# Optimization experiments

Hardware: AMD Instinct MI355X
Metric: run time of the kernel (lower is better)

## Reference

```python
import jax, jax.numpy as jnp
import numpy as np

NUM_TYPES = 4  # unique atom types, e.g. H,C,N,O
N_DESC = 384   # descriptor width (nDescriptors())


def setup_inputs() -> dict:
    key = jax.random.key(0)
    k1, k2, k3 = jax.random.split(key, 3)
    n_confs, n_atoms = 2048, 64
    coords = jax.random.normal(k1, (n_confs, n_atoms, 3), dtype=jnp.float32)
    atom_types = jax.random.randint(k2, (n_confs, n_atoms), 0, NUM_TYPES, dtype=jnp.int64)
    W = jax.random.normal(k3, (3, N_DESC), dtype=jnp.float32)
    return {"coords": coords, "atom_types": atom_types, "W": W}


def reference(coords, atom_types, W):
    n_confs, n_atoms, _ = coords.shape
    # stub descriptor computer: per-atom descriptor, (n_confs*n_atoms, N_DESC)
    desc = jnp.tanh(coords.reshape(-1, 3) @ W)
    at2type = atom_types.reshape(-1)                      # (N,)
    # conformer index for every atom: [0,0,...,0,1,1,...]
    at2conf = jnp.repeat(jnp.arange(n_confs, dtype=jnp.int64), n_atoms)
    # stable sort by atom type (routing permutation)
    perm = jnp.argsort(at2type, stable=True)              # (N,)
    desc_sorted = desc[perm]                              # gather (N, N_DESC)
    at2conf_sorted = at2conf[perm]                        # (N,)
    at_type_count = jnp.bincount(at2type, length=NUM_TYPES)  # split sizes per type
    # per-type buckets = desc_sorted split at cumsum(at_type_count); returned
    # concatenated with counts to keep shapes static under jit.
    return desc_sorted, at2conf_sorted, at_type_count
```

## Files before the change

### kernel.cpp

```cpp
#include <hip/hip_runtime.h>

#define NDESC 384
#define NTYPES 4
#define BLOCK_ATOMS 256
#define NTHREADS 384

typedef unsigned int uint32;
typedef unsigned long long u64;
typedef float f4 __attribute__((ext_vector_type(4)));

__device__ __forceinline__ float fast_tanh(float x) {
  float e = __builtin_amdgcn_exp2f(x * 2.8853900817779268f);
  return 1.0f - 2.0f * __builtin_amdgcn_rcpf(1.0f + e);
}

__global__ __launch_bounds__(BLOCK_ATOMS) void hist_kernel(
    const int* __restrict__ types, uint32* __restrict__ blockHist, int n) {
  __shared__ uint32 waveCnt[BLOCK_ATOMS / 64][NTYPES];
  int tid = threadIdx.x;
  int idx = blockIdx.x * BLOCK_ATOMS + tid;
  int ty = (idx < n) ? types[idx] : -1;
  int wave = tid >> 6, lane = tid & 63;
  for (int t = 0; t < NTYPES; ++t) {
    u64 m = __ballot(ty == t);
    if (lane == 0) waveCnt[wave][t] = (uint32)__popcll(m);
  }
  __syncthreads();
  if (tid < NTYPES) {
    uint32 s = 0;
    for (int w = 0; w < BLOCK_ATOMS / 64; ++w) s += waveCnt[w][tid];
    blockHist[blockIdx.x * NTYPES + tid] = s;
  }
}

__global__ __launch_bounds__(NTHREADS) void main_kernel(
    const float* __restrict__ coords, const int* __restrict__ types,
    const float* __restrict__ W, const uint32* __restrict__ blockHist,
    float* __restrict__ descOut, float* __restrict__ confOut,
    float* __restrict__ countsOut, int n, int nb) {
  __shared__ float sW[3 * NDESC];
  __shared__ float sC[BLOCK_ATOMS][3];
  __shared__ uint32 sRankPos[BLOCK_ATOMS];
  __shared__ uint32 sRankAtom[BLOCK_ATOMS];
  __shared__ uint32 waveCnt[BLOCK_ATOMS / 64][NTYPES];
  __shared__ uint32 sTot[NTYPES];
  __shared__ uint32 sOff[NTYPES];
  __shared__ uint32 sCum[NTYPES];

  int tid = threadIdx.x;
  int bid = blockIdx.x;
  int base = bid * BLOCK_ATOMS;

  for (int i = tid; i < 3 * NDESC; i += NTHREADS) sW[i] = W[i];
  for (int i = tid; i < BLOCK_ATOMS * 3; i += NTHREADS) {
    int g = base * 3 + i;
    sC[i / 3][i % 3] = (g < n * 3) ? coords[g] : 0.0f;
  }

  int idx = base + tid;
  int ty = -1;
  if (tid < BLOCK_ATOMS && idx < n) ty = types[idx];
  int wave = tid >> 6, lane = tid & 63;
  int myrank = 0;
  if (tid < BLOCK_ATOMS) {
    for (int t = 0; t < NTYPES; ++t) {
      u64 m = __ballot(ty == t);
      if (lane == 0) waveCnt[wave][t] = (uint32)__popcll(m);
      if (t == ty) myrank = (int)__popcll(m & ((1ull << lane) - 1ull));
    }
  }

  if (wave < NTYPES) {
    int t = wave;
    uint32 tot = 0, pre = 0;
    for (int b = lane; b < nb; b += 64) {
      uint32 h = blockHist[b * NTYPES + t];
      tot += h;
      if (b < bid) pre += h;
    }
    for (int off = 32; off > 0; off >>= 1) {
      tot += __shfl_down(tot, off);
      pre += __shfl_down(pre, off);
    }
    if (lane == 0) { sTot[t] = tot; sOff[t] = pre; }
  }
  __syncthreads();
  if (tid == 0) {
    uint32 b = 0, c = 0;
    for (int t = 0; t < NTYPES; ++t) {
      sOff[t] += b;
      b += sTot[t];
      uint32 cnt = 0;
      for (int w = 0; w < BLOCK_ATOMS / 64; ++w) cnt += waveCnt[w][t];
      sCum[t] = c;
      c += cnt;
    }
  }
  if (bid == 0 && tid < NTYPES) countsOut[tid] = (float)sTot[tid];
  __syncthreads();

  if (tid < BLOCK_ATOMS && ty >= 0) {
    uint32 fullrank = (uint32)myrank;
    for (int w = 0; w < wave; ++w) fullrank += waveCnt[w][ty];
    uint32 pos = sOff[ty] + fullrank;
    uint32 brk = sCum[ty] + fullrank;
    sRankPos[brk] = pos;
    sRankAtom[brk] = (uint32)tid;
    confOut[pos] = (float)(idx >> 6);
  }
  __syncthreads();

  int r = tid / 96;
  int c = tid - r * 96;
  int d0 = 4 * c;
  float w00 = sW[d0], w01 = sW[d0 + 1], w02 = sW[d0 + 2], w03 = sW[d0 + 3];
  float w10 = sW[NDESC + d0], w11 = sW[NDESC + d0 + 1],
        w12 = sW[NDESC + d0 + 2], w13 = sW[NDESC + d0 + 3];
  float w20 = sW[2 * NDESC + d0], w21 = sW[2 * NDESC + d0 + 1],
        w22 = sW[2 * NDESC + d0 + 2], w23 = sW[2 * NDESC + d0 + 3];

  int valid = n - base;
  if (valid > BLOCK_ATOMS) valid = BLOCK_ATOMS;

  if (valid == BLOCK_ATOMS) {
#pragma unroll 8
    for (int k0 = 0; k0 < BLOCK_ATOMS; k0 += 4) {
      int k = k0 + r;
      uint32 a = sRankAtom[k];
      uint32 pos = sRankPos[k];
      float c0 = sC[a][0], c1 = sC[a][1], c2 = sC[a][2];
      f4 v;
      v.x = fast_tanh(c0 * w00 + c1 * w10 + c2 * w20);
      v.y = fast_tanh(c0 * w01 + c1 * w11 + c2 * w21);
      v.z = fast_tanh(c0 * w02 + c1 * w12 + c2 * w22);
      v.w = fast_tanh(c0 * w03 + c1 * w13 + c2 * w23);
      __builtin_nontemporal_store(
          v, reinterpret_cast<f4*>(descOut + (size_t)pos * NDESC + d0));
    }
  } else {
    for (int k0 = 0; k0 < BLOCK_ATOMS; k0 += 4) {
      int k = k0 + r;
      if (k < valid) {
        uint32 a = sRankAtom[k];
        uint32 pos = sRankPos[k];
        float c0 = sC[a][0], c1 = sC[a][1], c2 = sC[a][2];
        f4 v;
        v.x = fast_tanh(c0 * w00 + c1 * w10 + c2 * w20);
        v.y = fast_tanh(c0 * w01 + c1 * w11 + c2 * w21);
        v.z = fast_tanh(c0 * w02 + c1 * w12 + c2 * w22);
        v.w = fast_tanh(c0 * w03 + c1 * w13 + c2 * w23);
        __builtin_nontemporal_store(
            v, reinterpret_cast<f4*>(descOut + (size_t)pos * NDESC + d0));
      }
    }
  }
}

extern "C" void kernel_launch(void* const* d_in, const int* in_sizes, int n_in,
                              void* d_out, int out_size, void* d_ws, size_t ws_size,
                              hipStream_t stream) {
  const float* coords = (const float*)d_in[0];
  const int* types = (const int*)d_in[1];
  const float* W = (const float*)d_in[2];

  int n = in_sizes[1];
  int nb = (n + BLOCK_ATOMS - 1) / BLOCK_ATOMS;

  uint32* blockHist = (uint32*)d_ws;

  float* descOut = (float*)d_out;
  float* confOut = descOut + (size_t)n * NDESC;
  float* countsOut = confOut + n;

  hipLaunchKernelGGL(hist_kernel, dim3(nb), dim3(BLOCK_ATOMS), 0, stream,
                     types, blockHist, n);
  hipLaunchKernelGGL(main_kernel, dim3(nb), dim3(NTHREADS), 0, stream,
                     coords, types, W, blockHist, descOut, confOut, countsOut,
                     n, nb);
}
```

Baseline: 53.71 us.

## Split scatter into permutation kernel plus contiguous gather-compute kernel

```diff
diff --git a/kernel.cpp b/kernel.cpp
--- a/kernel.cpp
+++ b/kernel.cpp
@@ -4,6 +4,7 @@
 #define NTYPES 4
 #define BLOCK_ATOMS 256
 #define NTHREADS 384
+#define ROWS 64
 
 typedef unsigned int uint32;
 typedef unsigned long long u64;
@@ -33,41 +34,24 @@
   }
 }
 
-__global__ __launch_bounds__(NTHREADS) void main_kernel(
-    const float* __restrict__ coords, const int* __restrict__ types,
-    const float* __restrict__ W, const uint32* __restrict__ blockHist,
-    float* __restrict__ descOut, float* __restrict__ confOut,
-    float* __restrict__ countsOut, int n, int nb) {
-  __shared__ float sW[3 * NDESC];
-  __shared__ float sC[BLOCK_ATOMS][3];
-  __shared__ uint32 sRankPos[BLOCK_ATOMS];
-  __shared__ uint32 sRankAtom[BLOCK_ATOMS];
+__global__ __launch_bounds__(BLOCK_ATOMS) void perm_kernel(
+    const int* __restrict__ types, const uint32* __restrict__ blockHist,
+    uint32* __restrict__ perm, float* __restrict__ countsOut, int n, int nb) {
   __shared__ uint32 waveCnt[BLOCK_ATOMS / 64][NTYPES];
   __shared__ uint32 sTot[NTYPES];
   __shared__ uint32 sOff[NTYPES];
-  __shared__ uint32 sCum[NTYPES];
 
   int tid = threadIdx.x;
   int bid = blockIdx.x;
   int base = bid * BLOCK_ATOMS;
-
-  for (int i = tid; i < 3 * NDESC; i += NTHREADS) sW[i] = W[i];
-  for (int i = tid; i < BLOCK_ATOMS * 3; i += NTHREADS) {
-    int g = base * 3 + i;
-    sC[i / 3][i % 3] = (g < n * 3) ? coords[g] : 0.0f;
-  }
-
   int idx = base + tid;
-  int ty = -1;
-  if (tid < BLOCK_ATOMS && idx < n) ty = types[idx];
+  int ty = (idx < n) ? types[idx] : -1;
   int wave = tid >> 6, lane = tid & 63;
   int myrank = 0;
-  if (tid < BLOCK_ATOMS) {
-    for (int t = 0; t < NTYPES; ++t) {
-      u64 m = __ballot(ty == t);
-      if (lane == 0) waveCnt[wave][t] = (uint32)__popcll(m);
-      if (t == ty) myrank = (int)__popcll(m & ((1ull << lane) - 1ull));
-    }
+  for (int t = 0; t < NTYPES; ++t) {
+    u64 m = __ballot(ty == t);
+    if (lane == 0) waveCnt[wave][t] = (uint32)__popcll(m);
+    if (t == ty) myrank = (int)__popcll(m & ((1ull << lane) - 1ull));
   }
 
   if (wave < NTYPES) {
@@ -86,27 +70,42 @@
   }
   __syncthreads();
   if (tid == 0) {
-    uint32 b = 0, c = 0;
-    for (int t = 0; t < NTYPES; ++t) {
-      sOff[t] += b;
-      b += sTot[t];
-      uint32 cnt = 0;
-      for (int w = 0; w < BLOCK_ATOMS / 64; ++w) cnt += waveCnt[w][t];
-      sCum[t] = c;
-      c += cnt;
-    }
+    uint32 b = 0;
+    for (int t = 0; t < NTYPES; ++t) { sOff[t] += b; b += sTot[t]; }
   }
   if (bid == 0 && tid < NTYPES) countsOut[tid] = (float)sTot[tid];
   __syncthreads();
 
-  if (tid < BLOCK_ATOMS && ty >= 0) {
+  if (ty >= 0) {
     uint32 fullrank = (uint32)myrank;
     for (int w = 0; w < wave; ++w) fullrank += waveCnt[w][ty];
-    uint32 pos = sOff[ty] + fullrank;
-    uint32 brk = sCum[ty] + fullrank;
-    sRankPos[brk] = pos;
-    sRankAtom[brk] = (uint32)tid;
-    confOut[pos] = (float)(idx >> 6);
+    perm[sOff[ty] + fullrank] = (uint32)idx;
+  }
+}
+
+__global__ __launch_bounds__(NTHREADS) void gather_kernel(
+    const float* __restrict__ coords, const uint32* __restrict__ perm,
+    const float* __restrict__ W, float* __restrict__ descOut,
+    float* __restrict__ confOut, int n) {
+  __shared__ float sW[3 * NDESC];
+  __shared__ float sC[ROWS][3];
+  __shared__ uint32 sPerm[ROWS];
+
+  int tid = threadIdx.x;
+  int base = blockIdx.x * ROWS;
+
+  for (int i = tid; i < 3 * NDESC; i += NTHREADS) sW[i] = W[i];
+  if (tid < ROWS) {
+    int p = base + tid;
+    uint32 a = (p < n) ? perm[p] : 0u;
+    sPerm[tid] = a;
+    if (p < n) confOut[p] = (float)(a >> 6);
+  }
+  __syncthreads();
+  if (tid < ROWS * 3) {
+    int rrow = tid / 3, comp = tid - 3 * rrow;
+    sC[rrow][comp] = (base + rrow < n)
+                         ? coords[(size_t)sPerm[rrow] * 3 + comp] : 0.0f;
   }
   __syncthreads();
 
@@ -120,37 +119,31 @@
         w22 = sW[2 * NDESC + d0 + 2], w23 = sW[2 * NDESC + d0 + 3];
 
   int valid = n - base;
-  if (valid > BLOCK_ATOMS) valid = BLOCK_ATOMS;
+  if (valid > ROWS) valid = ROWS;
 
-  if (valid == BLOCK_ATOMS) {
-#pragma unroll 8
-    for (int k0 = 0; k0 < BLOCK_ATOMS; k0 += 4) {
+  if (valid == ROWS) {
+#pragma unroll 4
+    for (int k0 = 0; k0 < ROWS; k0 += 4) {
       int k = k0 + r;
-      uint32 a = sRankAtom[k];
-      uint32 pos = sRankPos[k];
-      float c0 = sC[a][0], c1 = sC[a][1], c2 = sC[a][2];
+      float c0 = sC[k][0], c1 = sC[k][1], c2 = sC[k][2];
       f4 v;
       v.x = fast_tanh(c0 * w00 + c1 * w10 + c2 * w20);
       v.y = fast_tanh(c0 * w01 + c1 * w11 + c2 * w21);
       v.z = fast_tanh(c0 * w02 + c1 * w12 + c2 * w22);
       v.w = fast_tanh(c0 * w03 + c1 * w13 + c2 * w23);
-      __builtin_nontemporal_store(
-          v, reinterpret_cast<f4*>(descOut + (size_t)pos * NDESC + d0));
+      *reinterpret_cast<f4*>(descOut + (size_t)(base + k) * NDESC + d0) = v;
     }
   } else {
-    for (int k0 = 0; k0 < BLOCK_ATOMS; k0 += 4) {
+    for (int k0 = 0; k0 < ROWS; k0 += 4) {
       int k = k0 + r;
       if (k < valid) {
-        uint32 a = sRankAtom[k];
-        uint32 pos = sRankPos[k];
-        float c0 = sC[a][0], c1 = sC[a][1], c2 = sC[a][2];
+        float c0 = sC[k][0], c1 = sC[k][1], c2 = sC[k][2];
         f4 v;
         v.x = fast_tanh(c0 * w00 + c1 * w10 + c2 * w20);
         v.y = fast_tanh(c0 * w01 + c1 * w11 + c2 * w21);
         v.z = fast_tanh(c0 * w02 + c1 * w12 + c2 * w22);
         v.w = fast_tanh(c0 * w03 + c1 * w13 + c2 * w23);
-        __builtin_nontemporal_store(
-            v, reinterpret_cast<f4*>(descOut + (size_t)pos * NDESC + d0));
+        *reinterpret_cast<f4*>(descOut + (size_t)(base + k) * NDESC + d0) = v;
       }
     }
   }
@@ -165,8 +158,10 @@
 
   int n = in_sizes[1];
   int nb = (n + BLOCK_ATOMS - 1) / BLOCK_ATOMS;
+  int ngb = (n + ROWS - 1) / ROWS;
 
   uint32* blockHist = (uint32*)d_ws;
+  uint32* perm = blockHist + (size_t)nb * NTYPES;
 
   float* descOut = (float*)d_out;
   float* confOut = descOut + (size_t)n * NDESC;
@@ -174,7 +169,8 @@
 
   hipLaunchKernelGGL(hist_kernel, dim3(nb), dim3(BLOCK_ATOMS), 0, stream,
                      types, blockHist, n);
-  hipLaunchKernelGGL(main_kernel, dim3(nb), dim3(NTHREADS), 0, stream,
-                     coords, types, W, blockHist, descOut, confOut, countsOut,
-                     n, nb);
+  hipLaunchKernelGGL(perm_kernel, dim3(nb), dim3(BLOCK_ATOMS), 0, stream,
+                     types, blockHist, perm, countsOut, n, nb);
+  hipLaunchKernelGGL(gather_kernel, dim3(ngb), dim3(NTHREADS), 0, stream,
+                     coords, perm, W, descOut, confOut, n);
 }
```

After: 48.39 us. 1.11x faster.
